# Optimization experiments

Hardware: AMD Instinct MI355X
Metric: run time of the kernel (lower is better)

The kernel has to match this reference:

```python
import jax, jax.numpy as jnp
import numpy as np

B = 4096          # batch_size * world_size
D = 256           # embedding dim
TEMP = 0.5        # temperature
EPS = 1e-8


def setup_inputs() -> dict:
    key = jax.random.key(0)
    k1, k2 = jax.random.split(key)
    z_i = jax.random.normal(k1, (B, D), dtype=jnp.float32)
    z_j = jax.random.normal(k2, (B, D), dtype=jnp.float32)
    return {"z_i": z_i, "z_j": z_j}


def reference(z_i, z_j):
    N = 2 * B
    z = jnp.concatenate([z_i, z_j], axis=0)                      # [N, D]
    # cosine similarity = normalized dot products (normalize + GEMM)
    norm = jnp.sqrt(jnp.sum(z * z, axis=-1, keepdims=True))
    zn = z / jnp.maximum(norm, EPS)
    sim = (zn @ zn.T) / TEMP                                     # [N, N]
    # positives: pairs (i, i+B) and (i+B, i)
    idx = jnp.arange(N)
    pos = sim[idx, (idx + B) % N]                                # [N]
    # CE with label 0 over [pos, negatives]; the candidate set equals the
    # full sim row minus the diagonal (pos is re-included), so:
    sim_masked = jnp.where(jnp.eye(N, dtype=bool), -jnp.inf, sim)
    lse = jax.nn.logsumexp(sim_masked, axis=1)                   # [N]
    loss = jnp.sum(lse - pos) / N                                # reduction='sum' then /N
    return loss
```

## Files before the change

kernel.cpp:

```cpp
#include <hip/hip_runtime.h>
#include <hip/hip_bf16.h>
#include <cmath>

#define B_SZ 4096
#define N_SZ 8192
#define D_SZ 256
#define EPS 1e-8f
#define EXPC 0.01127105500694503f
#define EXPB -2.8853900817779268f

typedef __attribute__((ext_vector_type(4))) float f32x4;
typedef __attribute__((ext_vector_type(4))) int   i32x4;
typedef __attribute__((ext_vector_type(8))) int   i32x8;

__device__ __forceinline__ void dma16(const void* g, void* l) {
    __builtin_amdgcn_global_load_lds(
        (const __attribute__((address_space(1))) unsigned int*)g,
        (__attribute__((address_space(3))) unsigned int*)l, 16, 0, 0);
}


__global__ __launch_bounds__(256) void prep_kernel(const float* __restrict__ zi,
                                                   const float* __restrict__ zj,
                                                   char* __restrict__ znb,
                                                   float* __restrict__ pos,
                                                   float* __restrict__ accf,
                                                   unsigned* __restrict__ counter) {
    if (blockIdx.x == 0 && threadIdx.x == 0) { *accf = 0.0f; *counter = 0u; }
    const int wave = threadIdx.x >> 6, lane = threadIdx.x & 63;
    const int i = blockIdx.x * 4 + wave;
    float4 a = reinterpret_cast<const float4*>(zi + (size_t)i * D_SZ)[lane];
    float4 b = reinterpret_cast<const float4*>(zj + (size_t)i * D_SZ)[lane];
    float ssa = a.x * a.x + a.y * a.y + a.z * a.z + a.w * a.w;
    float ssb = b.x * b.x + b.y * b.y + b.z * b.z + b.w * b.w;
    float dab = a.x * b.x + a.y * b.y + a.z * b.z + a.w * b.w;
    #pragma unroll
    for (int off = 32; off; off >>= 1) {
        ssa += __shfl_xor(ssa, off, 64);
        ssb += __shfl_xor(ssb, off, 64);
        dab += __shfl_xor(dab, off, 64);
    }
    const float invna = 1.0f / fmaxf(sqrtf(ssa), EPS);
    const float invnb = 1.0f / fmaxf(sqrtf(ssb), EPS);
    if (lane == 0) {
        float p = dab * invna * invnb * 2.0f;
        pos[i] = p;
        pos[i + B_SZ] = p;
    }
    const float sa = invna * 16.0f, sb = invnb * 16.0f;
    const int koff = (lane >> 2) * 1024 + (lane & 3) * 4;
    {
        int pk = __builtin_amdgcn_cvt_pk_fp8_f32(a.x * sa, a.y * sa, 0, false);
        pk     = __builtin_amdgcn_cvt_pk_fp8_f32(a.z * sa, a.w * sa, pk, true);
        *reinterpret_cast<int*>(znb + (size_t)(i >> 6) * 16384 + koff + (i & 63) * 16) = pk;
    }
    {
        const int r = i + B_SZ;
        int pk = __builtin_amdgcn_cvt_pk_fp8_f32(b.x * sb, b.y * sb, 0, false);
        pk     = __builtin_amdgcn_cvt_pk_fp8_f32(b.z * sb, b.w * sb, pk, true);
        *reinterpret_cast<int*>(znb + (size_t)(r >> 6) * 16384 + koff + (r & 63) * 16) = pk;
    }
}

__global__ __launch_bounds__(512, 4) void simlse_kernel(const char* __restrict__ znb,
                                                        float* __restrict__ partial) {
    __shared__ __attribute__((aligned(16))) char blds[65536];
    __shared__ float cs[8][256];

    const int t = threadIdx.x;
    const int wave = t >> 6, lane = t & 63;

    int bid = blockIdx.x, rt = 0;
    #pragma unroll 1
    for (; rt < 32; ++rt) {
        int cnt = 32 - rt;
        if (bid < cnt) break;
        bid -= cnt;
    }
    const int chunk = rt + bid;
    const bool offdiag = (rt != chunk);

    const int rl = lane & 15;
    const int kg = lane >> 4;
    const int i0 = rt * 256 + wave * 32;

    {
        const char* gp = znb + (size_t)chunk * 65536 + t * 16;
        char* lp = blds + t * 16;
        #pragma unroll
        for (int c = 0; c < 8; ++c) dma16(gp + c * 8192, lp + c * 8192);
    }

    const char* ap = znb + (size_t)(rt * 4 + (wave >> 1)) * 16384 +
                     (wave & 1) * 512 + rl * 16;
    i32x8 afrag[2][2];
    #pragma unroll
    for (int g = 0; g < 2; ++g)
        #pragma unroll
        for (int kc = 0; kc < 2; ++kc) {
            i32x4 lo = *reinterpret_cast<const i32x4*>(
                ap + (kc * 8 + kg * 2) * 1024 + g * 256);
            i32x4 hi = *reinterpret_cast<const i32x4*>(
                ap + (kc * 8 + kg * 2 + 1) * 1024 + g * 256);
            afrag[g][kc] = __builtin_shufflevector(lo, hi, 0, 1, 2, 3, 4, 5, 6, 7);
        }

    float s_acc[2][4];
    #pragma unroll
    for (int g = 0; g < 2; ++g)
        #pragma unroll
        for (int r = 0; r < 4; ++r) s_acc[g][r] = 0.0f;

    const char* bp0 = blds + kg * 2048 + rl * 16;

    i32x8 bf0, bf1;
    f32x4 accA[2], accB[2];

    #define PREP_B(F)                                                             \
        {                                                                         \
            const char* bq = bp0 + ((F) >> 2) * 16384 + ((F) & 3) * 256;          \
            i32x4 l0 = *reinterpret_cast<const i32x4*>(bq);                       \
            i32x4 l1 = *reinterpret_cast<const i32x4*>(bq + 1024);                \
            i32x4 l2 = *reinterpret_cast<const i32x4*>(bq + 8192);                \
            i32x4 l3 = *reinterpret_cast<const i32x4*>(bq + 9216);                \
            bf0 = __builtin_shufflevector(l0, l1, 0, 1, 2, 3, 4, 5, 6, 7);        \
            bf1 = __builtin_shufflevector(l2, l3, 0, 1, 2, 3, 4, 5, 6, 7);        \
        }

    #define MFMA4(ACC)                                                            \
        {                                                                         \
            _Pragma("unroll")                                                     \
            for (int g = 0; g < 2; ++g) ACC[g] = (f32x4){0.f, 0.f, 0.f, 0.f};     \
            _Pragma("unroll")                                                     \
            for (int g = 0; g < 2; ++g)                                           \
                asm("v_mfma_f32_16x16x128_f8f6f4 %0, %1, %2, %0"                  \
                    : "+v"(ACC[g]) : "v"(afrag[g][0]), "v"(bf0));                 \
            _Pragma("unroll")                                                     \
            for (int g = 0; g < 2; ++g)                                           \
                asm("v_mfma_f32_16x16x128_f8f6f4 %0, %1, %2, %0"                  \
                    : "+v"(ACC[g]) : "v"(afrag[g][1]), "v"(bf1));                 \
        }

    #define EXPSUM(ACC, F)                                                        \
        {                                                                         \
            float cthr = 0.0f;                                                    \
            _Pragma("unroll")                                                     \
            for (int g = 0; g < 2; ++g)                                           \
                _Pragma("unroll")                                                 \
                for (int r = 0; r < 4; ++r) {                                     \
                    float e = __builtin_amdgcn_exp2f(fmaf(ACC[g][r], EXPC, EXPB)); \
                    s_acc[g][r] += e;                                             \
                    cthr += e;                                                    \
                }                                                                 \
            cthr += __shfl_xor(cthr, 16, 64);                                     \
            cthr += __shfl_xor(cthr, 32, 64);                                     \
            if (offdiag && lane < 16)                                             \
                cs[wave][((F) >> 2) * 64 + ((F) & 3) * 16 + rl] = cthr;           \
        }

    __syncthreads();

    PREP_B(0);
    MFMA4(accA);
    #pragma unroll 1
    for (int fo = 0; fo < 7; ++fo) {
        const int f1 = 2 * fo + 1, f2 = 2 * fo + 2;
        PREP_B(f1); MFMA4(accB);
        asm volatile("s_nop 7");
        EXPSUM(accA, f1 - 1);
        PREP_B(f2); MFMA4(accA);
        asm volatile("s_nop 7");
        EXPSUM(accB, f2 - 1);
    }
    PREP_B(15); MFMA4(accB);
    asm volatile("s_nop 7");
    EXPSUM(accA, 14);
    asm volatile("s_nop 7");
    EXPSUM(accB, 15);

    #pragma unroll
    for (int g = 0; g < 2; ++g)
        #pragma unroll
        for (int r = 0; r < 4; ++r) {
            float v = s_acc[g][r];
            #pragma unroll
            for (int off = 1; off < 16; off <<= 1) v += __shfl_xor(v, off, 64);
            if (rl == 0)
                partial[chunk * N_SZ + i0 + g * 16 + kg * 4 + r] = v;
        }

    if (offdiag) {
        __syncthreads();
        if (t < 256) {
            float v = 0.0f;
            #pragma unroll
            for (int w = 0; w < 8; ++w) v += cs[w][t];
            partial[rt * N_SZ + chunk * 256 + t] = v;
        }
    }
    #undef PREP_B
    #undef MFMA4
    #undef EXPSUM
}

__global__ __launch_bounds__(256) void rowsum_kernel(const float* __restrict__ partial,
                                                     const float* __restrict__ pos,
                                                     float* __restrict__ accf,
                                                     unsigned* __restrict__ counter,
                                                     float* __restrict__ out) {
    const int row = blockIdx.x * 256 + threadIdx.x;
    float s = -1.0f;
    #pragma unroll
    for (int c = 0; c < 32; ++c) s += partial[c * N_SZ + row];
    float acc = 2.0f + logf(s) - pos[row];
    #pragma unroll
    for (int off = 32; off; off >>= 1) acc += __shfl_xor(acc, off, 64);
    __shared__ float w[4];
    if ((threadIdx.x & 63) == 0) w[threadIdx.x >> 6] = acc;
    __syncthreads();
    if (threadIdx.x == 0) {
        atomicAdd(accf, w[0] + w[1] + w[2] + w[3]);
        __threadfence();
        unsigned old = atomicAdd(counter, 1u);
        if (old == 31u) {
            float tot = atomicAdd(accf, 0.0f);
            out[0] = tot / (float)N_SZ;
        }
    }
}

extern "C" void kernel_launch(void* const* d_in, const int* in_sizes, int n_in,
                              void* d_out, int out_size, void* d_ws, size_t ws_size,
                              hipStream_t stream) {
    const float* zi = (const float*)d_in[0];
    const float* zj = (const float*)d_in[1];

    char* ws = (char*)d_ws;
    char* znb       = ws;
    float* pos      = (float*)(ws + 2097152);
    float* partial  = (float*)(ws + 2097152 + 32768);
    float* accf     = (float*)(ws + 2097152 + 32768 + 1048576);
    unsigned* counter = (unsigned*)(ws + 2097152 + 32768 + 1048576 + 4);
    float* out = (float*)d_out;

    prep_kernel<<<B_SZ / 4, 256, 0, stream>>>(zi, zj, znb, pos, accf, counter);
    simlse_kernel<<<528, 512, 0, stream>>>(znb, partial);
    rowsum_kernel<<<32, 256, 0, stream>>>(partial, pos, accf, counter, out);
}
```

Before: 32.92 us.

## Fuse row-sum reduction into sim kernel via global tile counter spin-wait

Removes the separate rowsum kernel launch. Every sim/LSE block bumps a global tiles_done counter after storing its partials, and the first 32 blocks spin until all 528 tiles finish before doing the final log-sum reduction. Control words are now cleared with a hipMemsetAsync instead of inside prep. MFMA issue is also wrapped in s_setprio raises. The spin-wait relies on all blocks being co-resident or making progress, and it adds a memset launch.

```diff
diff --git a/kernel.cpp b/kernel.cpp
--- a/kernel.cpp
+++ b/kernel.cpp
@@ -8,6 +8,7 @@
 #define EPS 1e-8f
 #define EXPC 0.01127105500694503f
 #define EXPB -2.8853900817779268f
+#define NTILE 528u
 
 typedef __attribute__((ext_vector_type(4))) float f32x4;
 typedef __attribute__((ext_vector_type(4))) int   i32x4;
@@ -19,14 +20,18 @@
         (__attribute__((address_space(3))) unsigned int*)l, 16, 0, 0);
 }
 
+__device__ __forceinline__ void agent_store(float* p, float v) {
+    __hip_atomic_store(p, v, __ATOMIC_RELAXED, __HIP_MEMORY_SCOPE_AGENT);
+}
+__device__ __forceinline__ float agent_load(const float* p) {
+    return __hip_atomic_load(p, __ATOMIC_RELAXED, __HIP_MEMORY_SCOPE_AGENT);
+}
+
 
 __global__ __launch_bounds__(256) void prep_kernel(const float* __restrict__ zi,
                                                    const float* __restrict__ zj,
                                                    char* __restrict__ znb,
-                                                   float* __restrict__ pos,
-                                                   float* __restrict__ accf,
-                                                   unsigned* __restrict__ counter) {
-    if (blockIdx.x == 0 && threadIdx.x == 0) { *accf = 0.0f; *counter = 0u; }
+                                                   float* __restrict__ pos) {
     const int wave = threadIdx.x >> 6, lane = threadIdx.x & 63;
     const int i = blockIdx.x * 4 + wave;
     float4 a = reinterpret_cast<const float4*>(zi + (size_t)i * D_SZ)[lane];
@@ -62,8 +67,13 @@
     }
 }
 
-__global__ __launch_bounds__(512, 4) void simlse_kernel(const char* __restrict__ znb,
-                                                        float* __restrict__ partial) {
+__global__ __launch_bounds__(512, 4) void fused_kernel(const char* __restrict__ znb,
+                                                       const float* __restrict__ pos,
+                                                       float* __restrict__ partial,
+                                                       unsigned* __restrict__ tiles_done,
+                                                       float* __restrict__ accf,
+                                                       unsigned* __restrict__ counter2,
+                                                       float* __restrict__ out) {
     __shared__ __attribute__((aligned(16))) char blds[65536];
     __shared__ float cs[8][256];
 
@@ -131,6 +141,7 @@
         {                                                                         \
             _Pragma("unroll")                                                     \
             for (int g = 0; g < 2; ++g) ACC[g] = (f32x4){0.f, 0.f, 0.f, 0.f};     \
+            __builtin_amdgcn_s_setprio(1);                                        \
             _Pragma("unroll")                                                     \
             for (int g = 0; g < 2; ++g)                                           \
                 asm("v_mfma_f32_16x16x128_f8f6f4 %0, %1, %2, %0"                  \
@@ -139,6 +150,7 @@
             for (int g = 0; g < 2; ++g)                                           \
                 asm("v_mfma_f32_16x16x128_f8f6f4 %0, %1, %2, %0"                  \
                     : "+v"(ACC[g]) : "v"(afrag[g][1]), "v"(bf1));                 \
+            __builtin_amdgcn_s_setprio(0);                                        \
         }
 
     #define EXPSUM(ACC, F)                                                        \
@@ -186,7 +198,7 @@
             #pragma unroll
             for (int off = 1; off < 16; off <<= 1) v += __shfl_xor(v, off, 64);
             if (rl == 0)
-                partial[chunk * N_SZ + i0 + g * 16 + kg * 4 + r] = v;
+                agent_store(&partial[(size_t)chunk * N_SZ + i0 + g * 16 + kg * 4 + r], v);
         }
 
     if (offdiag) {
@@ -195,36 +207,46 @@
             float v = 0.0f;
             #pragma unroll
             for (int w = 0; w < 8; ++w) v += cs[w][t];
-            partial[rt * N_SZ + chunk * 256 + t] = v;
+            agent_store(&partial[(size_t)rt * N_SZ + chunk * 256 + t], v);
         }
     }
     #undef PREP_B
     #undef MFMA4
     #undef EXPSUM
-}
-
-__global__ __launch_bounds__(256) void rowsum_kernel(const float* __restrict__ partial,
-                                                     const float* __restrict__ pos,
-                                                     float* __restrict__ accf,
-                                                     unsigned* __restrict__ counter,
-                                                     float* __restrict__ out) {
-    const int row = blockIdx.x * 256 + threadIdx.x;
-    float s = -1.0f;
-    #pragma unroll
-    for (int c = 0; c < 32; ++c) s += partial[c * N_SZ + row];
-    float acc = 2.0f + logf(s) - pos[row];
-    #pragma unroll
-    for (int off = 32; off; off >>= 1) acc += __shfl_xor(acc, off, 64);
-    __shared__ float w[4];
-    if ((threadIdx.x & 63) == 0) w[threadIdx.x >> 6] = acc;
+
     __syncthreads();
-    if (threadIdx.x == 0) {
-        atomicAdd(accf, w[0] + w[1] + w[2] + w[3]);
+    if (t == 0) {
         __threadfence();
-        unsigned old = atomicAdd(counter, 1u);
-        if (old == 31u) {
-            float tot = atomicAdd(accf, 0.0f);
-            out[0] = tot / (float)N_SZ;
+        atomicAdd(tiles_done, 1u);
+    }
+
+    if (blockIdx.x < 32) {
+        if (t == 0) {
+            while (__hip_atomic_load(tiles_done, __ATOMIC_RELAXED,
+                                     __HIP_MEMORY_SCOPE_AGENT) < NTILE)
+                __builtin_amdgcn_s_sleep(32);
+            __threadfence();
+        }
+        __syncthreads();
+        float sacc = 0.0f;
+        if (t < 256) {
+            const int row = (int)blockIdx.x * 256 + t;
+            float s = -1.0f;
+            #pragma unroll 4
+            for (int c = 0; c < 32; ++c)
+                s += agent_load(&partial[(size_t)c * N_SZ + row]);
+            sacc = 2.0f + logf(s) - pos[row];
+            #pragma unroll
+            for (int off = 32; off; off >>= 1) sacc += __shfl_xor(sacc, off, 64);
+            if (lane == 0) cs[0][wave] = sacc;
+        }
+        __syncthreads();
+        if (t == 0) {
+            atomicAdd(accf, cs[0][0] + cs[0][1] + cs[0][2] + cs[0][3]);
+            __threadfence();
+            unsigned old = atomicAdd(counter2, 1u);
+            if (old == 31u)
+                out[0] = atomicAdd(accf, 0.0f) / (float)N_SZ;
         }
     }
 }
@@ -239,11 +261,14 @@
     char* znb       = ws;
     float* pos      = (float*)(ws + 2097152);
     float* partial  = (float*)(ws + 2097152 + 32768);
-    float* accf     = (float*)(ws + 2097152 + 32768 + 1048576);
-    unsigned* counter = (unsigned*)(ws + 2097152 + 32768 + 1048576 + 4);
+    char* ctrl      = ws + 2097152 + 32768 + 1048576;
+    unsigned* tiles_done = (unsigned*)ctrl;
+    unsigned* counter2   = (unsigned*)(ctrl + 4);
+    float* accf          = (float*)(ctrl + 8);
     float* out = (float*)d_out;
 
-    prep_kernel<<<B_SZ / 4, 256, 0, stream>>>(zi, zj, znb, pos, accf, counter);
-    simlse_kernel<<<528, 512, 0, stream>>>(znb, partial);
-    rowsum_kernel<<<32, 256, 0, stream>>>(partial, pos, accf, counter, out);
-}
+    hipMemsetAsync(ctrl, 0, 64, stream);
+    prep_kernel<<<B_SZ / 4, 256, 0, stream>>>(zi, zj, znb, pos);
+    fused_kernel<<<528, 512, 0, stream>>>(znb, pos, partial,
+                                          tiles_done, accf, counter2, out);
+}
```

New measurement: 54.10 us. 1.64x slower.

## Use 4-wave blocks with 64-row A tiles and two-stage B staging in LDS

Applied to the files above, without the earlier changes.

The similarity/LSE kernel moves from 8 waves × 32 rows to 4 waves × 64 rows per block. Each wave now reuses every B fragment across four MFMA groups instead of two. The B chunk is staged into LDS in two 32KB halves with a sync between them, which halves LDS use per block. The triangular tile mapping is also replaced by a closed-form pairing that balances work across blocks. The aim is better register-level reuse of B and lower LDS footprint, at the cost of more VGPRs, an extra barrier, and exposed latency on the second stage load.

```diff
diff --git a/kernel.cpp b/kernel.cpp
--- a/kernel.cpp
+++ b/kernel.cpp
@@ -62,40 +62,43 @@
     }
 }
 
-__global__ __launch_bounds__(512, 4) void simlse_kernel(const char* __restrict__ znb,
+__global__ __launch_bounds__(256, 3) void simlse_kernel(const char* __restrict__ znb,
                                                         float* __restrict__ partial) {
-    __shared__ __attribute__((aligned(16))) char blds[65536];
-    __shared__ float cs[8][256];
+    __shared__ __attribute__((aligned(16))) char blds[32768];
+    __shared__ float cs[4][256];
 
     const int t = threadIdx.x;
     const int wave = t >> 6, lane = t & 63;
 
-    int bid = blockIdx.x, rt = 0;
-    #pragma unroll 1
-    for (; rt < 32; ++rt) {
-        int cnt = 32 - rt;
-        if (bid < cnt) break;
-        bid -= cnt;
-    }
-    const int chunk = rt + bid;
+    int rt, chunk;
+    {
+        const int x = blockIdx.x & 7;
+        int j = blockIdx.x >> 3;
+        int p = x;
+        if (j >= 33) { j -= 33; p = x + 8; }
+        if (j <= p) { rt = j; chunk = p; }
+        else        { rt = j - (p + 1); chunk = 31 - p; }
+    }
     const bool offdiag = (rt != chunk);
 
     const int rl = lane & 15;
     const int kg = lane >> 4;
-    const int i0 = rt * 256 + wave * 32;
-
-    {
-        const char* gp = znb + (size_t)chunk * 65536 + t * 16;
-        char* lp = blds + t * 16;
-        #pragma unroll
-        for (int c = 0; c < 8; ++c) dma16(gp + c * 8192, lp + c * 8192);
-    }
-
-    const char* ap = znb + (size_t)(rt * 4 + (wave >> 1)) * 16384 +
-                     (wave & 1) * 512 + rl * 16;
-    i32x8 afrag[2][2];
-    #pragma unroll
-    for (int g = 0; g < 2; ++g)
+    const int i0 = rt * 256 + wave * 64;
+
+    #define STAGE(H)                                                              \
+        {                                                                         \
+            const char* gp = znb + (size_t)chunk * 65536 + (H) * 32768 + t * 16;  \
+            char* lp = blds + t * 16;                                             \
+            _Pragma("unroll")                                                     \
+            for (int c = 0; c < 8; ++c) dma16(gp + c * 4096, lp + c * 4096);      \
+        }
+
+    STAGE(0);
+
+    const char* ap = znb + (size_t)(rt * 4 + wave) * 16384 + rl * 16;
+    i32x8 afrag[4][2];
+    #pragma unroll
+    for (int g = 0; g < 4; ++g)
         #pragma unroll
         for (int kc = 0; kc < 2; ++kc) {
             i32x4 lo = *reinterpret_cast<const i32x4*>(
@@ -105,20 +108,20 @@
             afrag[g][kc] = __builtin_shufflevector(lo, hi, 0, 1, 2, 3, 4, 5, 6, 7);
         }
 
-    float s_acc[2][4];
-    #pragma unroll
-    for (int g = 0; g < 2; ++g)
+    float s_acc[4][4];
+    #pragma unroll
+    for (int g = 0; g < 4; ++g)
         #pragma unroll
         for (int r = 0; r < 4; ++r) s_acc[g][r] = 0.0f;
 
     const char* bp0 = blds + kg * 2048 + rl * 16;
 
     i32x8 bf0, bf1;
-    f32x4 accA[2], accB[2];
-
-    #define PREP_B(F)                                                             \
-        {                                                                         \
-            const char* bq = bp0 + ((F) >> 2) * 16384 + ((F) & 3) * 256;          \
+    f32x4 accA[4], accB[4];
+
+    #define LOADB(FL)                                                             \
+        {                                                                         \
+            const char* bq = bp0 + ((FL) >> 2) * 16384 + ((FL) & 3) * 256;        \
             i32x4 l0 = *reinterpret_cast<const i32x4*>(bq);                       \
             i32x4 l1 = *reinterpret_cast<const i32x4*>(bq + 1024);                \
             i32x4 l2 = *reinterpret_cast<const i32x4*>(bq + 8192);                \
@@ -127,16 +130,16 @@
             bf1 = __builtin_shufflevector(l2, l3, 0, 1, 2, 3, 4, 5, 6, 7);        \
         }
 
-    #define MFMA4(ACC)                                                            \
-        {                                                                         \
-            _Pragma("unroll")                                                     \
-            for (int g = 0; g < 2; ++g) ACC[g] = (f32x4){0.f, 0.f, 0.f, 0.f};     \
-            _Pragma("unroll")                                                     \
-            for (int g = 0; g < 2; ++g)                                           \
+    #define MFMA8(ACC)                                                            \
+        {                                                                         \
+            _Pragma("unroll")                                                     \
+            for (int g = 0; g < 4; ++g) ACC[g] = (f32x4){0.f, 0.f, 0.f, 0.f};     \
+            _Pragma("unroll")                                                     \
+            for (int g = 0; g < 4; ++g)                                           \
                 asm("v_mfma_f32_16x16x128_f8f6f4 %0, %1, %2, %0"                  \
                     : "+v"(ACC[g]) : "v"(afrag[g][0]), "v"(bf0));                 \
             _Pragma("unroll")                                                     \
-            for (int g = 0; g < 2; ++g)                                           \
+            for (int g = 0; g < 4; ++g)                                           \
                 asm("v_mfma_f32_16x16x128_f8f6f4 %0, %1, %2, %0"                  \
                     : "+v"(ACC[g]) : "v"(afrag[g][1]), "v"(bf1));                 \
         }
@@ -145,7 +148,7 @@
         {                                                                         \
             float cthr = 0.0f;                                                    \
             _Pragma("unroll")                                                     \
-            for (int g = 0; g < 2; ++g)                                           \
+            for (int g = 0; g < 4; ++g)                                           \
                 _Pragma("unroll")                                                 \
                 for (int r = 0; r < 4; ++r) {                                     \
                     float e = __builtin_amdgcn_exp2f(fmaf(ACC[g][r], EXPC, EXPB)); \
@@ -155,31 +158,50 @@
             cthr += __shfl_xor(cthr, 16, 64);                                     \
             cthr += __shfl_xor(cthr, 32, 64);                                     \
             if (offdiag && lane < 16)                                             \
-                cs[wave][((F) >> 2) * 64 + ((F) & 3) * 16 + rl] = cthr;           \
-        }
-
-    __syncthreads();
-
-    PREP_B(0);
-    MFMA4(accA);
+                cs[wave][(F) * 16 + rl] = cthr;                                   \
+        }
+
+    __syncthreads();
+
+    LOADB(0); MFMA8(accA);
     #pragma unroll 1
-    for (int fo = 0; fo < 7; ++fo) {
+    for (int fo = 0; fo < 3; ++fo) {
         const int f1 = 2 * fo + 1, f2 = 2 * fo + 2;
-        PREP_B(f1); MFMA4(accB);
+        LOADB(f1); MFMA8(accB);
         asm volatile("s_nop 7");
         EXPSUM(accA, f1 - 1);
-        PREP_B(f2); MFMA4(accA);
+        LOADB(f2); MFMA8(accA);
         asm volatile("s_nop 7");
         EXPSUM(accB, f2 - 1);
     }
-    PREP_B(15); MFMA4(accB);
+    LOADB(7); MFMA8(accB);
+    asm volatile("s_nop 7");
+    EXPSUM(accA, 6);
+
+    __syncthreads();
+    STAGE(1);
+    EXPSUM(accB, 7);
+    __syncthreads();
+
+    LOADB(0); MFMA8(accA);
+    #pragma unroll 1
+    for (int fo = 0; fo < 3; ++fo) {
+        const int f1 = 2 * fo + 1, f2 = 2 * fo + 2;
+        LOADB(f1); MFMA8(accB);
+        asm volatile("s_nop 7");
+        EXPSUM(accA, 8 + f1 - 1);
+        LOADB(f2); MFMA8(accA);
+        asm volatile("s_nop 7");
+        EXPSUM(accB, 8 + f2 - 1);
+    }
+    LOADB(7); MFMA8(accB);
     asm volatile("s_nop 7");
     EXPSUM(accA, 14);
     asm volatile("s_nop 7");
     EXPSUM(accB, 15);
 
     #pragma unroll
-    for (int g = 0; g < 2; ++g)
+    for (int g = 0; g < 4; ++g)
         #pragma unroll
         for (int r = 0; r < 4; ++r) {
             float v = s_acc[g][r];
@@ -191,15 +213,12 @@
 
     if (offdiag) {
         __syncthreads();
-        if (t < 256) {
-            float v = 0.0f;
-            #pragma unroll
-            for (int w = 0; w < 8; ++w) v += cs[w][t];
-            partial[rt * N_SZ + chunk * 256 + t] = v;
-        }
-    }
-    #undef PREP_B
-    #undef MFMA4
+        float v = cs[0][t] + cs[1][t] + cs[2][t] + cs[3][t];
+        partial[rt * N_SZ + chunk * 256 + t] = v;
+    }
+    #undef STAGE
+    #undef LOADB
+    #undef MFMA8
     #undef EXPSUM
 }
 
@@ -244,6 +263,6 @@
     float* out = (float*)d_out;
 
     prep_kernel<<<B_SZ / 4, 256, 0, stream>>>(zi, zj, znb, pos, accf, counter);
-    simlse_kernel<<<528, 512, 0, stream>>>(znb, partial);
+    simlse_kernel<<<528, 256, 0, stream>>>(znb, partial);
     rowsum_kernel<<<32, 256, 0, stream>>>(partial, pos, accf, counter, out);
 }
```

Measured after the change: 31.73 us. 3.6% less time.
